# Performance work log

Measured on AMD Instinct MI355X. Metric: run time of the kernel, lower is better.

The kernel has to match this reference:

```python
import jax, jax.numpy as jnp
import numpy as np

D_MODEL = 1024
N_HEADS = 16
D_HEAD = D_MODEL // N_HEADS
BLOCK = 2048
EPS = 1e-5


def layer_norm(x, w, b):
    mu = jnp.mean(x, axis=-1, keepdims=True)
    var = jnp.mean(jnp.square(x - mu), axis=-1, keepdims=True)
    return (x - mu) * jax.lax.rsqrt(var + EPS) * w + b


def setup_inputs() -> dict:
    key = jax.random.key(0)
    ks = jax.random.split(key, 8)
    d = D_MODEL
    s = 1.0 / np.sqrt(d)
    return {
        "x": jax.random.normal(ks[0], (2, 2048, d), dtype=jnp.float32),
        "ln1_w": jnp.ones((d,), jnp.float32),
        "ln1_b": jnp.zeros((d,), jnp.float32),
        "ln2_w": jnp.ones((d,), jnp.float32),
        "ln2_b": jnp.zeros((d,), jnp.float32),
        "qkv_w": jax.random.normal(ks[1], (3 * d, d), jnp.float32) * s,
        "o_w": jax.random.normal(ks[2], (d, d), jnp.float32) * s,
        "ffn_w1": jax.random.normal(ks[3], (4 * d, d), jnp.float32) * s,
        "ffn_b1": jnp.zeros((4 * d,), jnp.float32),
        "ffn_w2": jax.random.normal(ks[4], (d, 4 * d), jnp.float32) * (1.0 / np.sqrt(4 * d)),
        "ffn_b2": jnp.zeros((d,), jnp.float32),
    }


def reference(x, ln1_w, ln1_b, ln2_w, ln2_b, qkv_w, o_w, ffn_w1, ffn_b1, ffn_w2, ffn_b2):
    b, n, d = x.shape
    h = layer_norm(x, ln1_w, ln1_b)
    # qkv: (b, n, 3, H, Dh)
    qkv = (h @ qkv_w.T).reshape(b, n, 3, N_HEADS, D_HEAD)
    q, k, v = qkv[:, :, 0], qkv[:, :, 1], qkv[:, :, 2]  # (b, n, H, Dh)
    scale = 1.0 / np.sqrt(D_HEAD)
    s = jnp.einsum("bqhd,bkhd->bhqk", q, k) * scale
    mask = jnp.tril(jnp.ones((n, n), dtype=bool))
    s = jnp.where(mask, s, -jnp.inf)
    a = jax.nn.softmax(s, axis=-1)
    attn_out = jnp.einsum("bhqk,bkhd->bqhd", a, v).reshape(b, n, d)
    x = x + attn_out @ o_w.T
    h2 = layer_norm(x, ln2_w, ln2_b)
    ff = jax.nn.gelu(h2 @ ffn_w1.T + ffn_b1, approximate=False) @ ffn_w2.T + ffn_b2
    return x + ff
```

## Files before the change

### kernel.cpp

```cpp
#include <hip/hip_runtime.h>
#include <math.h>

#define D_MODEL 1024
#define N_HEADS 16
#define D_HEAD  64
#define SEQ     2048
#define BATCH   2
#define M_TOT   (BATCH*SEQ)
#define FFN_DIM 4096

typedef __attribute__((ext_vector_type(8))) short bf16x8;
typedef __attribute__((ext_vector_type(4))) float f32x4;
typedef __attribute__((ext_vector_type(8))) unsigned short u16x8;

__device__ __forceinline__ unsigned short f2bf(float f) {
  unsigned int u = __float_as_uint(f);
  return (unsigned short)((u + 0x7fffu + ((u >> 16) & 1u)) >> 16);
}
__device__ __forceinline__ unsigned short f2bf_trunc(float f) {
  return (unsigned short)(__float_as_uint(f) >> 16);
}
__device__ __forceinline__ float bf2f(unsigned short s) {
  return __uint_as_float(((unsigned int)s) << 16);
}

__device__ __forceinline__ void async_ld16(void* lds, const void* g) {
  __builtin_amdgcn_global_load_lds(
      (const __attribute__((address_space(1))) unsigned int*)g,
      (__attribute__((address_space(3))) unsigned int*)lds, 16, 0, 0);
}

__device__ __forceinline__ float gelu_exact(float x) {
  return 0.5f * x * (1.f + erff(x * 0.70710678118654752f));
}

__global__ __launch_bounds__(256) void cvt_all(const float* __restrict__ qkv_w,
    const float* __restrict__ o_w, const float* __restrict__ w1,
    const float* __restrict__ w2, unsigned short* __restrict__ dst) {
  const long MEGc = 1024*1024;
  long i = (long)(blockIdx.x*256 + threadIdx.x)*4;
  const float* src; long off;
  if (i < 3*MEGc)      { src = qkv_w; off = i; }
  else if (i < 4*MEGc) { src = o_w;  off = i - 3*MEGc; }
  else if (i < 8*MEGc) { src = w1;   off = i - 4*MEGc; }
  else                 { src = w2;   off = i - 8*MEGc; }
  float4 v = *(const float4*)(src + off);
  ushort4 o = { f2bf(v.x), f2bf(v.y), f2bf(v.z), f2bf(v.w) };
  *(ushort4*)(dst + i) = o;
}

__global__ __launch_bounds__(256) void ln_kernel(const float* __restrict__ x,
    const float* __restrict__ w, const float* __restrict__ b,
    unsigned short* __restrict__ out) {
  int row = blockIdx.x;
  const float* xr = x + (size_t)row * D_MODEL;
  int c = threadIdx.x * 4;
  float4 v = *(const float4*)(xr + c);
  float s = v.x + v.y + v.z + v.w;
  __shared__ float red[4];
  #pragma unroll
  for (int o = 32; o > 0; o >>= 1) s += __shfl_down(s, o, 64);
  int wave = threadIdx.x >> 6;
  if ((threadIdx.x & 63) == 0) red[wave] = s;
  __syncthreads();
  float mean = (red[0]+red[1]+red[2]+red[3]) * (1.f/D_MODEL);
  __syncthreads();
  float d0 = v.x-mean, d1 = v.y-mean, d2 = v.z-mean, d3 = v.w-mean;
  float s2 = d0*d0 + d1*d1 + d2*d2 + d3*d3;
  #pragma unroll
  for (int o = 32; o > 0; o >>= 1) s2 += __shfl_down(s2, o, 64);
  if ((threadIdx.x & 63) == 0) red[wave] = s2;
  __syncthreads();
  float var = (red[0]+red[1]+red[2]+red[3]) * (1.f/D_MODEL);
  float rs = rsqrtf(var + 1e-5f);
  float4 wv = *(const float4*)(w + c);
  float4 bv = *(const float4*)(b + c);
  ushort4 o = { f2bf(d0*rs*wv.x + bv.x), f2bf(d1*rs*wv.y + bv.y),
                f2bf(d2*rs*wv.z + bv.z), f2bf(d3*rs*wv.w + bv.w) };
  *(ushort4*)(out + (size_t)row*D_MODEL + c) = o;
}

__device__ __forceinline__ void swizzle_block(int nbx, int nby, int& bx, int& by) {
  int nb = nbx * nby;
  int bid = blockIdx.y * nbx + blockIdx.x;
  int chunk = nb >> 3;
  int bid2 = (bid & 7) * chunk + (bid >> 3);
  const int GM = 8;
  int ngroup = GM * nbx;
  int g = bid2 / ngroup, rem = bid2 % ngroup;
  by = g*GM + (rem % GM);
  bx = rem / GM;
}

template<int EPI, bool OBF, int BN>
__global__ __launch_bounds__(128) void gemm_mfma(
    const unsigned short* __restrict__ A, const unsigned short* __restrict__ Bt,
    float* __restrict__ Cf, unsigned short* __restrict__ Cb,
    const float* __restrict__ bias, const float* __restrict__ res,
    int M, int N, int K) {
  constexpr int BM = 64, BK = 32;
  constexpr int TS = (BM + BN) * BK;
  constexpr int CPW = TS / 1024;
  constexpr int MI = (BN == 128) ? 4 : 2;
  __shared__ unsigned short Ls[2][TS];
  int tid = threadIdx.x;
  int w = tid >> 6, l = tid & 63;
  int lg = l >> 4, lm = l & 15;
  int bx, by;
  swizzle_block(N/BN, M/BM, bx, by);
  int bm = by * BM, bn = bx * BN;
  int wm = (BN == 128) ? 0 : w*32;
  int wn = (BN == 128) ? w*64 : 0;

  f32x4 acc[MI][4];
  #pragma unroll
  for (int i = 0; i < MI; ++i)
    #pragma unroll
    for (int j = 0; j < 4; ++j)
      acc[i][j] = (f32x4){0.f, 0.f, 0.f, 0.f};

  int swz = (l >> 3) & 3;
  const unsigned short* gp[CPW];
  int lo[CPW];
  #pragma unroll
  for (int cc = 0; cc < CPW; ++cc) {
    int c = w*CPW + cc;
    int r = c*16 + (l >> 2);
    int col = ((l & 3) ^ swz) * 8;
    lo[cc] = c*512 + l*8;
    gp[cc] = (r < BM) ? (A  + (size_t)(bm + r)*K + col)
                      : (Bt + (size_t)(bn + (r - BM))*K + col);
  }
  auto stage = [&](int buf, int k0) {
    #pragma unroll
    for (int cc = 0; cc < CPW; ++cc)
      async_ld16(&Ls[buf][lo[cc]], gp[cc] + k0);
  };

  int lgs = lg ^ ((lm >> 1) & 3);
  int aoff = (wm + lm)*BK + lgs*8;
  int boff = BM*BK + (wn + lm)*BK + lgs*8;

  stage(0, 0);
  int niter = K / BK;
  for (int kt = 0; kt < niter; ++kt) {
    __syncthreads();
    if (kt + 1 < niter) stage((kt+1) & 1, (kt+1)*BK);
    int buf = kt & 1;
    bf16x8 af[MI], bfr[4];
    #pragma unroll
    for (int i = 0; i < MI; ++i) af[i]  = *(const bf16x8*)&Ls[buf][aoff + i*512];
    #pragma unroll
    for (int j = 0; j < 4; ++j)  bfr[j] = *(const bf16x8*)&Ls[buf][boff + j*512];
    #pragma unroll
    for (int i = 0; i < MI; ++i)
      #pragma unroll
      for (int j = 0; j < 4; ++j)
        acc[i][j] = __builtin_amdgcn_mfma_f32_16x16x32_bf16(af[i], bfr[j], acc[i][j], 0, 0, 0);
  }

  #pragma unroll
  for (int i = 0; i < MI; ++i) {
    #pragma unroll
    for (int j = 0; j < 4; ++j) {
      int col = bn + wn + j*16 + lm;
      #pragma unroll
      for (int r = 0; r < 4; ++r) {
        int row = bm + wm + i*16 + lg*4 + r;
        float v = acc[i][j][r];
        if (EPI == 1) v = gelu_exact(v + bias[col]);
        if (EPI == 2) v += res[(size_t)row*N + col];
        if (EPI == 3) v += bias[col] + res[(size_t)row*N + col];
        if (OBF) Cb[(size_t)row*N + col] = f2bf(v);
        else     Cf[(size_t)row*N + col] = v;
      }
    }
  }
}

__global__ __launch_bounds__(256) void vtrans_kernel(
    const unsigned short* __restrict__ qkvb, unsigned short* __restrict__ vT) {
  __shared__ unsigned short T[64*72];
  int nt = blockIdx.x, h = blockIdx.y, b = blockIdx.z;
  int tid = threadIdx.x;
  const unsigned short* vb = qkvb + (size_t)(b*SEQ)*(3*D_MODEL) + 2*D_MODEL + h*D_HEAD;
  #pragma unroll
  for (int it = 0; it < 2; ++it) {
    int idx = tid + it*256;
    int r = idx >> 3, c8 = (idx & 7)*8;
    *(u16x8*)&T[r*72 + c8] = *(const u16x8*)(vb + (size_t)(nt*64 + r)*(3*D_MODEL) + c8);
  }
  __syncthreads();
  unsigned short* vto = vT + ((size_t)(b*N_HEADS + h)*D_HEAD)*SEQ + nt*64;
  #pragma unroll
  for (int it = 0; it < 2; ++it) {
    int idx = tid + it*256;
    int d = idx >> 3, s8 = (idx & 7)*8;
    u16x8 o;
    #pragma unroll
    for (int i = 0; i < 8; ++i) o[i] = T[(s8+i)*72 + d];
    *(u16x8*)(vto + (size_t)d*SEQ + s8) = o;
  }
}

#define ATT_PAD 72
__device__ __forceinline__ void attn_step(
    const bf16x8* aq, float* m_i, float* l_i, f32x4* acc_o,
    const unsigned short* __restrict__ Ks, const unsigned short* __restrict__ Vt,
    unsigned short* __restrict__ pw, int lg, int lm, int qoff, bool diag) {
  f32x4 sacc[4];
  #pragma unroll
  for (int j = 0; j < 4; ++j) sacc[j] = (f32x4){0.f, 0.f, 0.f, 0.f};
  #pragma unroll
  for (int s = 0; s < 2; ++s)
    #pragma unroll
    for (int j = 0; j < 4; ++j)
      sacc[j] = __builtin_amdgcn_mfma_f32_16x16x32_bf16(
          aq[s], *(const bf16x8*)&Ks[(j*16+lm)*ATT_PAD + s*32 + lg*8], sacc[j], 0, 0, 0);
  if (diag) {
    #pragma unroll
    for (int j = 0; j < 4; ++j)
      #pragma unroll
      for (int r = 0; r < 4; ++r)
        if (j*16 + lm > qoff + lg*4 + r) sacc[j][r] = -INFINITY;
  }
  float alpha[4];
  #pragma unroll
  for (int r = 0; r < 4; ++r) {
    float rm = fmaxf(fmaxf(sacc[0][r], sacc[1][r]), fmaxf(sacc[2][r], sacc[3][r]));
    #pragma unroll
    for (int o = 1; o < 16; o <<= 1) rm = fmaxf(rm, __shfl_xor(rm, o));
    float mn = fmaxf(m_i[r], rm);
    alpha[r] = __expf(m_i[r] - mn);
    float rsum = 0.f;
    #pragma unroll
    for (int j = 0; j < 4; ++j) {
      float p = __expf(sacc[j][r] - mn);
      sacc[j][r] = p; rsum += p;
    }
    #pragma unroll
    for (int o = 1; o < 16; o <<= 1) rsum += __shfl_xor(rsum, o);
    l_i[r] = l_i[r]*alpha[r] + rsum;
    m_i[r] = mn;
  }
  #pragma unroll
  for (int j = 0; j < 4; ++j)
    #pragma unroll
    for (int r = 0; r < 4; ++r)
      pw[(lg*4 + r)*ATT_PAD + j*16 + lm] = f2bf_trunc(sacc[j][r]);
  #pragma unroll
  for (int j = 0; j < 4; ++j)
    #pragma unroll
    for (int r = 0; r < 4; ++r)
      acc_o[j][r] *= alpha[r];
  #pragma unroll
  for (int s = 0; s < 2; ++s) {
    bf16x8 ap = *(const bf16x8*)&pw[lm*ATT_PAD + s*32 + lg*8];
    #pragma unroll
    for (int j = 0; j < 4; ++j)
      acc_o[j] = __builtin_amdgcn_mfma_f32_16x16x32_bf16(
          ap, *(const bf16x8*)&Vt[(j*16+lm)*ATT_PAD + s*32 + lg*8], acc_o[j], 0, 0, 0);
  }
}

__global__ __launch_bounds__(256) void attn_mfma_kernel(
    const unsigned short* __restrict__ qkvb, const unsigned short* __restrict__ vT,
    unsigned short* __restrict__ out) {
  __shared__ unsigned short Ks[64*ATT_PAD];
  __shared__ unsigned short Vt[64*ATT_PAD];
  __shared__ unsigned short Pw[4][16*ATT_PAD];

  int pr = blockIdx.x, h = blockIdx.y, b = blockIdx.z;
  int qtH = 31 - pr, qtL = pr;
  int tid = threadIdx.x;
  int w = tid >> 6, l = tid & 63;
  int lg = l >> 4, lm = l & 15;

  const size_t rs3 = 3*D_MODEL;
  const unsigned short* qb  = qkvb + (size_t)(b*SEQ)*rs3 + h*D_HEAD;
  const unsigned short* kb  = qb + D_MODEL;
  const unsigned short* vtb = vT + ((size_t)(b*N_HEADS + h)*D_HEAD)*SEQ;

  bf16x8 aqH[2], aqL[2];
  int qrH = qtH*64 + w*16 + lm, qrL = qtL*64 + w*16 + lm;
  #pragma unroll
  for (int s = 0; s < 2; ++s) {
    u16x8 tH = *(const u16x8*)(qb + (size_t)qrH*rs3 + s*32 + lg*8);
    u16x8 tL = *(const u16x8*)(qb + (size_t)qrL*rs3 + s*32 + lg*8);
    bf16x8 rH, rL;
    #pragma unroll
    for (int i = 0; i < 8; ++i) {
      rH[i] = (short)f2bf(bf2f(tH[i]) * 0.125f);
      rL[i] = (short)f2bf(bf2f(tL[i]) * 0.125f);
    }
    aqH[s] = rH; aqL[s] = rL;
  }

  float mH[4], lH[4], mL[4], lL[4];
  f32x4 oH[4], oL[4];
  #pragma unroll
  for (int r = 0; r < 4; ++r) { mH[r] = -INFINITY; lH[r] = 0.f; mL[r] = -INFINITY; lL[r] = 0.f; }
  #pragma unroll
  for (int j = 0; j < 4; ++j) { oH[j] = (f32x4){0.f,0.f,0.f,0.f}; oL[j] = (f32x4){0.f,0.f,0.f,0.f}; }

  unsigned short* pw = &Pw[w][0];

  int sidx0 = tid, sidx1 = tid + 256;
  int sr0 = sidx0 >> 3, sc0 = (sidx0 & 7)*8;
  int sr1 = sidx1 >> 3, sc1 = (sidx1 & 7)*8;

  u16x8 kreg[2], vreg[2];
  auto prefetch = [&](int kt) {
    kreg[0] = *(const u16x8*)(kb  + (size_t)(kt*64 + sr0)*rs3 + sc0);
    kreg[1] = *(const u16x8*)(kb  + (size_t)(kt*64 + sr1)*rs3 + sc1);
    vreg[0] = *(const u16x8*)(vtb + (size_t)sr0*SEQ + kt*64 + sc0);
    vreg[1] = *(const u16x8*)(vtb + (size_t)sr1*SEQ + kt*64 + sc1);
  };

  prefetch(0);
  for (int kt = 0; kt <= qtH; ++kt) {
    __syncthreads();
    *(u16x8*)&Ks[sr0*ATT_PAD + sc0] = kreg[0];
    *(u16x8*)&Ks[sr1*ATT_PAD + sc1] = kreg[1];
    *(u16x8*)&Vt[sr0*ATT_PAD + sc0] = vreg[0];
    *(u16x8*)&Vt[sr1*ATT_PAD + sc1] = vreg[1];
    __syncthreads();
    if (kt < qtH) prefetch(kt+1);
    attn_step(aqH, mH, lH, oH, Ks, Vt, pw, lg, lm, w*16, kt == qtH);
    if (kt <= qtL)
      attn_step(aqL, mL, lL, oL, Ks, Vt, pw, lg, lm, w*16, kt == qtL);
  }

  #pragma unroll
  for (int r = 0; r < 4; ++r) {
    float invH = 1.f / lH[r], invL = 1.f / lL[r];
    int qH = qtH*64 + w*16 + lg*4 + r;
    int qL = qtL*64 + w*16 + lg*4 + r;
    #pragma unroll
    for (int j = 0; j < 4; ++j) {
      out[((size_t)(b*SEQ + qH))*D_MODEL + h*D_HEAD + j*16 + lm] = f2bf(oH[j][r]*invH);
      out[((size_t)(b*SEQ + qL))*D_MODEL + h*D_HEAD + j*16 + lm] = f2bf(oL[j][r]*invL);
    }
  }
}

extern "C" void kernel_launch(void* const* d_in, const int* in_sizes, int n_in,
                              void* d_out, int out_size, void* d_ws, size_t ws_size,
                              hipStream_t stream) {
  const float* x      = (const float*)d_in[0];
  const float* ln1_w  = (const float*)d_in[1];
  const float* ln1_b  = (const float*)d_in[2];
  const float* ln2_w  = (const float*)d_in[3];
  const float* ln2_b  = (const float*)d_in[4];
  const float* qkv_w  = (const float*)d_in[5];
  const float* o_w    = (const float*)d_in[6];
  const float* ffn_w1 = (const float*)d_in[7];
  const float* ffn_b1 = (const float*)d_in[8];
  const float* ffn_w2 = (const float*)d_in[9];
  const float* ffn_b2 = (const float*)d_in[10];
  float* out = (float*)d_out;
  float* ws  = (float*)d_ws;

  const size_t MEG = 1024*1024;
  unsigned short* wqkv = (unsigned short*)ws;
  unsigned short* wo   = wqkv + 3*MEG;
  unsigned short* w1   = wo   + 1*MEG;
  unsigned short* w2   = w1   + 4*MEG;
  unsigned short* hbf    = (unsigned short*)(ws + 6*MEG);
  unsigned short* attnbf = (unsigned short*)(ws + 8*MEG);
  float* x1  = ws + 10*MEG;
  unsigned short* qkvb = (unsigned short*)(ws + 14*MEG);
  unsigned short* ffbf = (unsigned short*)(ws + 14*MEG);
  unsigned short* vT   = (unsigned short*)(ws + 22*MEG);

  cvt_all<<<12*MEG/1024, 256, 0, stream>>>(qkv_w, o_w, ffn_w1, ffn_w2, wqkv);
  ln_kernel<<<M_TOT, 256, 0, stream>>>(x, ln1_w, ln1_b, hbf);
  gemm_mfma<0,true,128><<<dim3(3*D_MODEL/128, M_TOT/64), 128, 0, stream>>>(
      hbf, wqkv, nullptr, qkvb, nullptr, nullptr, M_TOT, 3*D_MODEL, D_MODEL);
  vtrans_kernel<<<dim3(SEQ/64, N_HEADS, BATCH), 256, 0, stream>>>(qkvb, vT);
  attn_mfma_kernel<<<dim3(16, N_HEADS, BATCH), 256, 0, stream>>>(qkvb, vT, attnbf);
  gemm_mfma<2,false,64><<<dim3(D_MODEL/64, M_TOT/64), 128, 0, stream>>>(
      attnbf, wo, x1, nullptr, nullptr, x, M_TOT, D_MODEL, D_MODEL);
  ln_kernel<<<M_TOT, 256, 0, stream>>>(x1, ln2_w, ln2_b, hbf);
  gemm_mfma<1,true,128><<<dim3(FFN_DIM/128, M_TOT/64), 128, 0, stream>>>(
      hbf, w1, nullptr, ffbf, ffn_b1, nullptr, M_TOT, FFN_DIM, D_MODEL);
  gemm_mfma<3,false,64><<<dim3(D_MODEL/64, M_TOT/64), 128, 0, stream>>>(
      ffbf, w2, out, nullptr, ffn_b2, x1, M_TOT, D_MODEL, FFN_DIM);
}
```

Before: 382.6 us.

## Use single-wave 64x64 GEMM tiles and drop barriers with vmcnt waits

The GEMM kernel now runs one 64-lane wavefront per block over a 64x64 tile, so each wave computes a 4x4 grid of MFMA tiles and issues all eight async loads per stage itself. Because only one wave touches shared memory, __syncthreads is replaced by s_waitcnt vmcnt counters, and the last iteration is peeled. This removes barrier overhead and makes the QKV and FFN1 GEMMs use square tiles with more blocks. The cost is fewer waves per block for latency hiding and more blocks competing for LDS.

```diff
diff --git a/kernel.cpp b/kernel.cpp
--- a/kernel.cpp
+++ b/kernel.cpp
@@ -92,81 +92,77 @@
   bx = rem / GM;
 }
 
-template<int EPI, bool OBF, int BN>
-__global__ __launch_bounds__(128) void gemm_mfma(
+template<int EPI, bool OBF>
+__global__ __launch_bounds__(64) void gemm_mfma(
     const unsigned short* __restrict__ A, const unsigned short* __restrict__ Bt,
     float* __restrict__ Cf, unsigned short* __restrict__ Cb,
     const float* __restrict__ bias, const float* __restrict__ res,
     int M, int N, int K) {
-  constexpr int BM = 64, BK = 32;
-  constexpr int TS = (BM + BN) * BK;
-  constexpr int CPW = TS / 1024;
-  constexpr int MI = (BN == 128) ? 4 : 2;
-  __shared__ unsigned short Ls[2][TS];
-  int tid = threadIdx.x;
-  int w = tid >> 6, l = tid & 63;
+  constexpr int BK = 32;
+  __shared__ unsigned short Ls[2][4096];
+  int l = threadIdx.x;
   int lg = l >> 4, lm = l & 15;
   int bx, by;
-  swizzle_block(N/BN, M/BM, bx, by);
-  int bm = by * BM, bn = bx * BN;
-  int wm = (BN == 128) ? 0 : w*32;
-  int wn = (BN == 128) ? w*64 : 0;
-
-  f32x4 acc[MI][4];
-  #pragma unroll
-  for (int i = 0; i < MI; ++i)
+  swizzle_block(N/64, M/64, bx, by);
+  int bm = by*64, bn = bx*64;
+
+  f32x4 acc[4][4];
+  #pragma unroll
+  for (int i = 0; i < 4; ++i)
     #pragma unroll
     for (int j = 0; j < 4; ++j)
       acc[i][j] = (f32x4){0.f, 0.f, 0.f, 0.f};
 
   int swz = (l >> 3) & 3;
-  const unsigned short* gp[CPW];
-  int lo[CPW];
-  #pragma unroll
-  for (int cc = 0; cc < CPW; ++cc) {
-    int c = w*CPW + cc;
+  const unsigned short* gp[8];
+  #pragma unroll
+  for (int c = 0; c < 8; ++c) {
     int r = c*16 + (l >> 2);
     int col = ((l & 3) ^ swz) * 8;
-    lo[cc] = c*512 + l*8;
-    gp[cc] = (r < BM) ? (A  + (size_t)(bm + r)*K + col)
-                      : (Bt + (size_t)(bn + (r - BM))*K + col);
+    gp[c] = (r < 64) ? (A  + (size_t)(bm + r)*K + col)
+                     : (Bt + (size_t)(bn + (r - 64))*K + col);
   }
   auto stage = [&](int buf, int k0) {
     #pragma unroll
-    for (int cc = 0; cc < CPW; ++cc)
-      async_ld16(&Ls[buf][lo[cc]], gp[cc] + k0);
+    for (int c = 0; c < 8; ++c)
+      async_ld16(&Ls[buf][c*512 + l*8], gp[c] + k0);
   };
 
   int lgs = lg ^ ((lm >> 1) & 3);
-  int aoff = (wm + lm)*BK + lgs*8;
-  int boff = BM*BK + (wn + lm)*BK + lgs*8;
-
-  stage(0, 0);
-  int niter = K / BK;
-  for (int kt = 0; kt < niter; ++kt) {
-    __syncthreads();
-    if (kt + 1 < niter) stage((kt+1) & 1, (kt+1)*BK);
-    int buf = kt & 1;
-    bf16x8 af[MI], bfr[4];
-    #pragma unroll
-    for (int i = 0; i < MI; ++i) af[i]  = *(const bf16x8*)&Ls[buf][aoff + i*512];
+  int aoff = lm*32 + lgs*8;
+  int boff = 2048 + lm*32 + lgs*8;
+
+  auto compute = [&](int buf) {
+    bf16x8 af[4], bfr[4];
+    #pragma unroll
+    for (int i = 0; i < 4; ++i) af[i]  = *(const bf16x8*)&Ls[buf][aoff + i*512];
     #pragma unroll
     for (int j = 0; j < 4; ++j)  bfr[j] = *(const bf16x8*)&Ls[buf][boff + j*512];
     #pragma unroll
-    for (int i = 0; i < MI; ++i)
+    for (int i = 0; i < 4; ++i)
       #pragma unroll
       for (int j = 0; j < 4; ++j)
         acc[i][j] = __builtin_amdgcn_mfma_f32_16x16x32_bf16(af[i], bfr[j], acc[i][j], 0, 0, 0);
-  }
-
-  #pragma unroll
-  for (int i = 0; i < MI; ++i) {
+  };
+
+  stage(0, 0);
+  int niter = K / BK;
+  for (int kt = 0; kt < niter - 1; ++kt) {
+    stage((kt+1) & 1, (kt+1)*BK);
+    asm volatile("s_waitcnt vmcnt(8)" ::: "memory");
+    compute(kt & 1);
+  }
+  asm volatile("s_waitcnt vmcnt(0)" ::: "memory");
+  compute((niter-1) & 1);
+
+  #pragma unroll
+  for (int i = 0; i < 4; ++i) {
     #pragma unroll
     for (int j = 0; j < 4; ++j) {
-      int col = bn + wn + j*16 + lm;
+      int col = bn + j*16 + lm;
       #pragma unroll
       for (int r = 0; r < 4; ++r) {
-        int row = bm + wm + i*16 + lg*4 + r;
+        int row = bm + i*16 + lg*4 + r;
         float v = acc[i][j][r];
         if (EPI == 1) v = gelu_exact(v + bias[col]);
         if (EPI == 2) v += res[(size_t)row*N + col];
@@ -375,15 +371,15 @@
 
   cvt_all<<<12*MEG/1024, 256, 0, stream>>>(qkv_w, o_w, ffn_w1, ffn_w2, wqkv);
   ln_kernel<<<M_TOT, 256, 0, stream>>>(x, ln1_w, ln1_b, hbf);
-  gemm_mfma<0,true,128><<<dim3(3*D_MODEL/128, M_TOT/64), 128, 0, stream>>>(
+  gemm_mfma<0,true><<<dim3(3*D_MODEL/64, M_TOT/64), 64, 0, stream>>>(
       hbf, wqkv, nullptr, qkvb, nullptr, nullptr, M_TOT, 3*D_MODEL, D_MODEL);
   vtrans_kernel<<<dim3(SEQ/64, N_HEADS, BATCH), 256, 0, stream>>>(qkvb, vT);
   attn_mfma_kernel<<<dim3(16, N_HEADS, BATCH), 256, 0, stream>>>(qkvb, vT, attnbf);
-  gemm_mfma<2,false,64><<<dim3(D_MODEL/64, M_TOT/64), 128, 0, stream>>>(
+  gemm_mfma<2,false><<<dim3(D_MODEL/64, M_TOT/64), 64, 0, stream>>>(
       attnbf, wo, x1, nullptr, nullptr, x, M_TOT, D_MODEL, D_MODEL);
   ln_kernel<<<M_TOT, 256, 0, stream>>>(x1, ln2_w, ln2_b, hbf);
-  gemm_mfma<1,true,128><<<dim3(FFN_DIM/128, M_TOT/64), 128, 0, stream>>>(
+  gemm_mfma<1,true><<<dim3(FFN_DIM/64, M_TOT/64), 64, 0, stream>>>(
       hbf, w1, nullptr, ffbf, ffn_b1, nullptr, M_TOT, FFN_DIM, D_MODEL);
-  gemm_mfma<3,false,64><<<dim3(D_MODEL/64, M_TOT/64), 128, 0, stream>>>(
+  gemm_mfma<3,false><<<dim3(D_MODEL/64, M_TOT/64), 64, 0, stream>>>(
       ffbf, w2, out, nullptr, ffn_b2, x1, M_TOT, D_MODEL, FFN_DIM);
 }
```

After: 446.5 us. +16.7%, slower.

## Enlarge GEMM tiles to 128-row blocks with 4 waves and register-staged prefetch

Applied to the files above, without the earlier changes.

Raises the GEMM block tile from 64 rows to 128 rows and uses 256 threads, so each of the four waves computes a 64xBN/2 sub-tile. This cuts redundant global loads per output and raises reuse of each shared-memory tile. It also replaces the async global-to-LDS loads with register prefetch: the next tile is loaded into registers, MFMA runs on the current tile, then the registers are written to LDS. In exchange it uses more registers and LDS per block and launches fewer blocks, which lowers occupancy and may leave CUs underfilled on the smaller GEMMs.

```diff
diff --git a/kernel.cpp b/kernel.cpp
--- a/kernel.cpp
+++ b/kernel.cpp
@@ -22,12 +22,6 @@
 }
 __device__ __forceinline__ float bf2f(unsigned short s) {
   return __uint_as_float(((unsigned int)s) << 16);
-}
-
-__device__ __forceinline__ void async_ld16(void* lds, const void* g) {
-  __builtin_amdgcn_global_load_lds(
-      (const __attribute__((address_space(1))) unsigned int*)g,
-      (__attribute__((address_space(3))) unsigned int*)lds, 16, 0, 0);
 }
 
 __device__ __forceinline__ float gelu_exact(float x) {
@@ -93,15 +87,15 @@
 }
 
 template<int EPI, bool OBF, int BN>
-__global__ __launch_bounds__(128) void gemm_mfma(
+__global__ __launch_bounds__(256) void gemm_mfma(
     const unsigned short* __restrict__ A, const unsigned short* __restrict__ Bt,
     float* __restrict__ Cf, unsigned short* __restrict__ Cb,
     const float* __restrict__ bias, const float* __restrict__ res,
     int M, int N, int K) {
-  constexpr int BM = 64, BK = 32;
+  constexpr int BM = 128, BK = 32;
   constexpr int TS = (BM + BN) * BK;
-  constexpr int CPW = TS / 1024;
-  constexpr int MI = (BN == 128) ? 4 : 2;
+  constexpr int CPT = TS / 2048;
+  constexpr int NI = (BN == 128) ? 4 : 2;
   __shared__ unsigned short Ls[2][TS];
   int tid = threadIdx.x;
   int w = tid >> 6, l = tid & 63;
@@ -109,60 +103,72 @@
   int bx, by;
   swizzle_block(N/BN, M/BM, bx, by);
   int bm = by * BM, bn = bx * BN;
-  int wm = (BN == 128) ? 0 : w*32;
-  int wn = (BN == 128) ? w*64 : 0;
-
-  f32x4 acc[MI][4];
-  #pragma unroll
-  for (int i = 0; i < MI; ++i)
-    #pragma unroll
-    for (int j = 0; j < 4; ++j)
+  int wm = (w >> 1) * 64;
+  int wn = (w & 1) * (BN/2);
+
+  f32x4 acc[4][NI];
+  #pragma unroll
+  for (int i = 0; i < 4; ++i)
+    #pragma unroll
+    for (int j = 0; j < NI; ++j)
       acc[i][j] = (f32x4){0.f, 0.f, 0.f, 0.f};
 
-  int swz = (l >> 3) & 3;
-  const unsigned short* gp[CPW];
-  int lo[CPW];
-  #pragma unroll
-  for (int cc = 0; cc < CPW; ++cc) {
-    int c = w*CPW + cc;
-    int r = c*16 + (l >> 2);
-    int col = ((l & 3) ^ swz) * 8;
-    lo[cc] = c*512 + l*8;
-    gp[cc] = (r < BM) ? (A  + (size_t)(bm + r)*K + col)
-                      : (Bt + (size_t)(bn + (r - BM))*K + col);
-  }
-  auto stage = [&](int buf, int k0) {
-    #pragma unroll
-    for (int cc = 0; cc < CPW; ++cc)
-      async_ld16(&Ls[buf][lo[cc]], gp[cc] + k0);
+  const unsigned short* gp[CPT];
+  int lo[CPT];
+  #pragma unroll
+  for (int i = 0; i < CPT; ++i) {
+    int fc = i*256 + tid;
+    int r = fc >> 2;
+    int swz = (fc >> 3) & 3;
+    int col = ((fc & 3) ^ swz) * 8;
+    lo[i] = fc * 8;
+    gp[i] = (r < BM) ? (A  + (size_t)(bm + r)*K + col)
+                     : (Bt + (size_t)(bn + (r - BM))*K + col);
+  }
+  u16x8 sreg[CPT];
+  auto loadregs = [&](int k0) {
+    #pragma unroll
+    for (int i = 0; i < CPT; ++i) sreg[i] = *(const u16x8*)(gp[i] + k0);
+  };
+  auto dswrite = [&](int buf) {
+    #pragma unroll
+    for (int i = 0; i < CPT; ++i) *(u16x8*)&Ls[buf][lo[i]] = sreg[i];
   };
 
   int lgs = lg ^ ((lm >> 1) & 3);
   int aoff = (wm + lm)*BK + lgs*8;
   int boff = BM*BK + (wn + lm)*BK + lgs*8;
 
-  stage(0, 0);
+  auto compute = [&](int buf) {
+    bf16x8 af[4], bfr[NI];
+    #pragma unroll
+    for (int i = 0; i < 4; ++i)  af[i]  = *(const bf16x8*)&Ls[buf][aoff + i*512];
+    #pragma unroll
+    for (int j = 0; j < NI; ++j) bfr[j] = *(const bf16x8*)&Ls[buf][boff + j*512];
+    #pragma unroll
+    for (int i = 0; i < 4; ++i)
+      #pragma unroll
+      for (int j = 0; j < NI; ++j)
+        acc[i][j] = __builtin_amdgcn_mfma_f32_16x16x32_bf16(af[i], bfr[j], acc[i][j], 0, 0, 0);
+  };
+
+  loadregs(0);
+  dswrite(0);
+  __syncthreads();
   int niter = K / BK;
   for (int kt = 0; kt < niter; ++kt) {
-    __syncthreads();
-    if (kt + 1 < niter) stage((kt+1) & 1, (kt+1)*BK);
-    int buf = kt & 1;
-    bf16x8 af[MI], bfr[4];
-    #pragma unroll
-    for (int i = 0; i < MI; ++i) af[i]  = *(const bf16x8*)&Ls[buf][aoff + i*512];
-    #pragma unroll
-    for (int j = 0; j < 4; ++j)  bfr[j] = *(const bf16x8*)&Ls[buf][boff + j*512];
-    #pragma unroll
-    for (int i = 0; i < MI; ++i)
-      #pragma unroll
-      for (int j = 0; j < 4; ++j)
-        acc[i][j] = __builtin_amdgcn_mfma_f32_16x16x32_bf16(af[i], bfr[j], acc[i][j], 0, 0, 0);
-  }
-
-  #pragma unroll
-  for (int i = 0; i < MI; ++i) {
-    #pragma unroll
-    for (int j = 0; j < 4; ++j) {
+    if (kt + 1 < niter) loadregs((kt+1)*BK);
+    compute(kt & 1);
+    if (kt + 1 < niter) {
+      dswrite((kt+1) & 1);
+      __syncthreads();
+    }
+  }
+
+  #pragma unroll
+  for (int i = 0; i < 4; ++i) {
+    #pragma unroll
+    for (int j = 0; j < NI; ++j) {
       int col = bn + wn + j*16 + lm;
       #pragma unroll
       for (int r = 0; r < 4; ++r) {
@@ -375,15 +381,15 @@
 
   cvt_all<<<12*MEG/1024, 256, 0, stream>>>(qkv_w, o_w, ffn_w1, ffn_w2, wqkv);
   ln_kernel<<<M_TOT, 256, 0, stream>>>(x, ln1_w, ln1_b, hbf);
-  gemm_mfma<0,true,128><<<dim3(3*D_MODEL/128, M_TOT/64), 128, 0, stream>>>(
+  gemm_mfma<0,true,128><<<dim3(3*D_MODEL/128, M_TOT/128), 256, 0, stream>>>(
       hbf, wqkv, nullptr, qkvb, nullptr, nullptr, M_TOT, 3*D_MODEL, D_MODEL);
   vtrans_kernel<<<dim3(SEQ/64, N_HEADS, BATCH), 256, 0, stream>>>(qkvb, vT);
   attn_mfma_kernel<<<dim3(16, N_HEADS, BATCH), 256, 0, stream>>>(qkvb, vT, attnbf);
-  gemm_mfma<2,false,64><<<dim3(D_MODEL/64, M_TOT/64), 128, 0, stream>>>(
+  gemm_mfma<2,false,64><<<dim3(D_MODEL/64, M_TOT/128), 256, 0, stream>>>(
       attnbf, wo, x1, nullptr, nullptr, x, M_TOT, D_MODEL, D_MODEL);
   ln_kernel<<<M_TOT, 256, 0, stream>>>(x1, ln2_w, ln2_b, hbf);
-  gemm_mfma<1,true,128><<<dim3(FFN_DIM/128, M_TOT/64), 128, 0, stream>>>(
+  gemm_mfma<1,true,128><<<dim3(FFN_DIM/128, M_TOT/128), 256, 0, stream>>>(
       hbf, w1, nullptr, ffbf, ffn_b1, nullptr, M_TOT, FFN_DIM, D_MODEL);
-  gemm_mfma<3,false,64><<<dim3(D_MODEL/64, M_TOT/64), 128, 0, stream>>>(
+  gemm_mfma<3,false,64><<<dim3(D_MODEL/64, M_TOT/128), 256, 0, stream>>>(
       ffbf, w2, out, nullptr, ffn_b2, x1, M_TOT, D_MODEL, FFN_DIM);
 }
```

After: 377.2 us. Within noise of the previous version (-1.4%).
